# Optimization experiments

Measured on AMD Instinct MI355X. Metric: run time of the kernel, lower is better.

The kernel has to match this reference:

```python
import jax, jax.numpy as jnp
import numpy as np

HEADS = 8

def setup_inputs() -> dict:
    key = jax.random.key(0)
    ks = jax.random.split(key, 6)
    B, HW, C = 8, 1024, 640  # B = b * num_frames, b=1, t=8
    s = 1.0 / np.sqrt(C)
    return {
        "hidden_states": jax.random.normal(ks[0], (B, HW, C), jnp.float32),
        "Wq": jax.random.normal(ks[1], (C, C), jnp.float32) * s,
        "Wk": jax.random.normal(ks[2], (C, C), jnp.float32) * s,
        "Wv": jax.random.normal(ks[3], (C, C), jnp.float32) * s,
        "Wo": jax.random.normal(ks[4], (C, C), jnp.float32) * s,
        "bo": jax.random.normal(ks[5], (C,), jnp.float32) * 0.01,
        "vision_conditon_frames_sample_index": jnp.zeros((1,), jnp.int64 if jax.config.jax_enable_x64 else jnp.int32),
        "num_frames": 8,
    }

def reference(hidden_states, Wq, Wk, Wv, Wo, bo, vision_conditon_frames_sample_index, num_frames):
    B, HW, C = hidden_states.shape
    dh = C // HEADS
    b = B // num_frames
    # (b t) hw c -> b t hw c
    ehs = hidden_states.reshape(b, num_frames, HW, C)
    # gather reference frames: b t_ref hw c -> b 1 (t_ref hw) c, repeat across t
    ip = jnp.take(ehs, vision_conditon_frames_sample_index, axis=1)
    ip = ip.reshape(b, 1, -1, C)
    ip = jnp.broadcast_to(ip, (b, num_frames, ip.shape[2], C))
    # concat per-frame tokens with reference tokens -> (b t) kv c
    ehs = jnp.concatenate([ehs, ip], axis=2).reshape(B, -1, C)
    KV = ehs.shape[1]
    # projections (LoRACompatibleLinear, no bias for q/k/v)
    q = (hidden_states @ Wq).reshape(B, HW, HEADS, dh)
    k = (ehs @ Wk).reshape(B, KV, HEADS, dh)
    v = (ehs @ Wv).reshape(B, KV, HEADS, dh)
    scale = 1.0 / np.sqrt(dh).astype(np.float32)
    logits = jnp.einsum("bqhd,bkhd->bhqk", q, k) * scale
    attn = jax.nn.softmax(logits, axis=-1)
    out = jnp.einsum("bhqk,bkhd->bqhd", attn, v).reshape(B, HW, C)
    # to_out[0] linear (with bias); dropout is identity at inference
    return out @ Wo + bo
```

## Files before the change

kernel.cpp:

```cpp
#include <hip/hip_runtime.h>

typedef __bf16 bf16x8 __attribute__((ext_vector_type(8)));
typedef float  f32x4  __attribute__((ext_vector_type(4)));
typedef unsigned short u16;

#define NFRM 8
#define HW   1024
#define CDIM 640
#define NH   8
#define DH   80

__device__ __forceinline__ u16 bfb(float f) {
    return __builtin_bit_cast(u16, (__bf16)f);
}

__global__ __launch_bounds__(256) void qkv_gemm(
    const float* __restrict__ hs, const float* __restrict__ Wq,
    const float* __restrict__ Wk, const float* __restrict__ Wv,
    u16* __restrict__ Qb, u16* __restrict__ Kb, u16* __restrict__ Vt)
{
    __shared__ u16 Al[128 * 40];
    __shared__ u16 Bl[64 * 40];

    const int m0 = blockIdx.x * 128;
    const int n0 = blockIdx.y * 64;
    const int z  = blockIdx.z;
    const float* __restrict__ W = (z == 0) ? Wq : (z == 1 ? Wk : Wv);

    const int t    = threadIdx.x;
    const int lane = t & 63, w = t >> 6;
    const int wm = w >> 1, wn = w & 1;
    const int g = lane >> 4, l16 = lane & 15;

    f32x4 acc[4][2] = {};

    const int ar = t >> 3;
    const int ac = (t & 7) * 4;

    for (int k0 = 0; k0 < CDIM; k0 += 32) {
        #pragma unroll
        for (int i = 0; i < 4; ++i) {
            int r = ar + i * 32;
            float4 v = *reinterpret_cast<const float4*>(hs + (size_t)(m0 + r) * CDIM + k0 + ac);
            ushort4 u;
            u.x = bfb(v.x); u.y = bfb(v.y); u.z = bfb(v.z); u.w = bfb(v.w);
            *reinterpret_cast<ushort4*>(&Al[r * 40 + ac]) = u;
        }
        #pragma unroll
        for (int i = 0; i < 2; ++i) {
            int nn = ac + i * 32;
            float4 v = *reinterpret_cast<const float4*>(W + (size_t)(k0 + ar) * CDIM + n0 + nn);
            Bl[(nn + 0) * 40 + ar] = bfb(v.x);
            Bl[(nn + 1) * 40 + ar] = bfb(v.y);
            Bl[(nn + 2) * 40 + ar] = bfb(v.z);
            Bl[(nn + 3) * 40 + ar] = bfb(v.w);
        }
        __syncthreads();

        bf16x8 af[4], bfr[2];
        #pragma unroll
        for (int mf = 0; mf < 4; ++mf)
            af[mf] = *reinterpret_cast<const bf16x8*>(&Al[(wm * 64 + mf * 16 + l16) * 40 + g * 8]);
        #pragma unroll
        for (int nf = 0; nf < 2; ++nf)
            bfr[nf] = *reinterpret_cast<const bf16x8*>(&Bl[(wn * 32 + nf * 16 + l16) * 40 + g * 8]);
        #pragma unroll
        for (int mf = 0; mf < 4; ++mf)
            #pragma unroll
            for (int nf = 0; nf < 2; ++nf)
                acc[mf][nf] = __builtin_amdgcn_mfma_f32_16x16x32_bf16(af[mf], bfr[nf], acc[mf][nf], 0, 0, 0);
        __syncthreads();
    }

    #pragma unroll
    for (int mf = 0; mf < 4; ++mf) {
        const int mrow0 = m0 + wm * 64 + mf * 16 + g * 4;
        const int b = mrow0 >> 10, tok0 = mrow0 & 1023;
        #pragma unroll
        for (int nf = 0; nf < 2; ++nf) {
            const int n = n0 + wn * 32 + nf * 16 + l16;
            const int h = n / DH, d = n % DH;
            if (z < 2) {
                u16* dst = (z == 0 ? Qb : Kb);
                size_t base = ((size_t)((b * NH + h) * HW) + tok0) * DH + d;
                #pragma unroll
                for (int rr = 0; rr < 4; ++rr)
                    dst[base + (size_t)rr * DH] = bfb(acc[mf][nf][rr]);
            } else {
                ushort4 u;
                u.x = bfb(acc[mf][nf][0]); u.y = bfb(acc[mf][nf][1]);
                u.z = bfb(acc[mf][nf][2]); u.w = bfb(acc[mf][nf][3]);
                *reinterpret_cast<ushort4*>(&Vt[((size_t)((b * NH + h) * DH) + d) * HW + tok0]) = u;
            }
        }
    }
}

__global__ __launch_bounds__(256) void attn_fwd(
    const u16* __restrict__ Qb, const u16* __restrict__ Kb,
    const u16* __restrict__ Vt, u16* __restrict__ Ob,
    const int* __restrict__ refidx)
{
    __shared__ u16 Kl[64 * 104];
    __shared__ u16 Vl[80 * 72];
    __shared__ u16 Pl[4][16 * 72];

    const int qt = blockIdx.x, h = blockIdx.y, b = blockIdx.z;
    const int t = threadIdx.x, lane = t & 63, w = t >> 6;
    const int g = lane >> 4, l16 = lane & 15;
    const int rfrm = refidx[0];
    const int qbase = qt * 64 + w * 16;

    const int srow = t >> 2;
    const int scol = (t & 3) * 24;

    {
        const u16* src = Qb + ((size_t)((b * NH + h) * HW) + qt * 64 + srow) * DH + scol;
        u16* dst = &Kl[srow * 104 + scol];
        #pragma unroll
        for (int i = 0; i < 3; ++i) {
            const int col = scol + i * 8;
            if (col < DH)
                *reinterpret_cast<uint4*>(dst + i * 8) = *reinterpret_cast<const uint4*>(src + i * 8);
            else
                *reinterpret_cast<uint4*>(dst + i * 8) = uint4{0, 0, 0, 0};
        }
    }
    __syncthreads();
    bf16x8 qf[3];
    #pragma unroll
    for (int s = 0; s < 3; ++s)
        qf[s] = *reinterpret_cast<const bf16x8*>(&Kl[(w * 16 + l16) * 104 + s * 32 + g * 8]);
    __syncthreads();

    float m_i[4], l_i[4];
    #pragma unroll
    for (int rr = 0; rr < 4; ++rr) { m_i[rr] = -1e30f; l_i[rr] = 0.f; }
    f32x4 o[5] = {};
    const float scale = 0.11180339887498948f;

    for (int kt = 0; kt < 32; ++kt) {
        const int fb   = (kt < 16) ? b : rfrm;
        const int tok0 = (kt & 15) * 64;

        {
            const u16* src = Kb + ((size_t)((fb * NH + h) * HW) + tok0 + srow) * DH + scol;
            u16* dst = &Kl[srow * 104 + scol];
            #pragma unroll
            for (int i = 0; i < 3; ++i) {
                const int col = scol + i * 8;
                if (col < DH)
                    *reinterpret_cast<uint4*>(dst + i * 8) = *reinterpret_cast<const uint4*>(src + i * 8);
                else
                    *reinterpret_cast<uint4*>(dst + i * 8) = uint4{0, 0, 0, 0};
            }
        }
        {
            const u16* Vp = Vt + (size_t)((fb * NH + h) * DH) * HW + tok0;
            #pragma unroll
            for (int i = 0; i < 3; ++i) {
                int id = t + i * 256;
                if (id < 640) {
                    int d = id >> 3, c = (id & 7) * 8;
                    *reinterpret_cast<uint4*>(&Vl[d * 72 + c]) =
                        *reinterpret_cast<const uint4*>(Vp + (size_t)d * HW + c);
                }
            }
        }
        __syncthreads();

        f32x4 s4[4] = {};
        #pragma unroll
        for (int nf = 0; nf < 4; ++nf) {
            #pragma unroll
            for (int s = 0; s < 3; ++s) {
                bf16x8 kf = *reinterpret_cast<const bf16x8*>(&Kl[(nf * 16 + l16) * 104 + s * 32 + g * 8]);
                s4[nf] = __builtin_amdgcn_mfma_f32_16x16x32_bf16(qf[s], kf, s4[nf], 0, 0, 0);
            }
        }

        float ps[4][4];
        #pragma unroll
        for (int nf = 0; nf < 4; ++nf)
            #pragma unroll
            for (int rr = 0; rr < 4; ++rr)
                ps[nf][rr] = s4[nf][rr] * scale;

        #pragma unroll
        for (int rr = 0; rr < 4; ++rr) {
            float mx = fmaxf(fmaxf(ps[0][rr], ps[1][rr]), fmaxf(ps[2][rr], ps[3][rr]));
            mx = fmaxf(mx, __shfl_xor(mx, 1));
            mx = fmaxf(mx, __shfl_xor(mx, 2));
            mx = fmaxf(mx, __shfl_xor(mx, 4));
            mx = fmaxf(mx, __shfl_xor(mx, 8));
            const float mnew = fmaxf(m_i[rr], mx);
            const float corr = __expf(m_i[rr] - mnew);
            m_i[rr] = mnew;
            float rsum = 0.f;
            #pragma unroll
            for (int nf = 0; nf < 4; ++nf) {
                float p = __expf(ps[nf][rr] - mnew);
                ps[nf][rr] = p;
                rsum += p;
            }
            rsum += __shfl_xor(rsum, 1);
            rsum += __shfl_xor(rsum, 2);
            rsum += __shfl_xor(rsum, 4);
            rsum += __shfl_xor(rsum, 8);
            l_i[rr] = l_i[rr] * corr + rsum;
            #pragma unroll
            for (int of = 0; of < 5; ++of)
                o[of][rr] = o[of][rr] * corr;
        }

        u16* Pw = &Pl[w][0];
        #pragma unroll
        for (int nf = 0; nf < 4; ++nf)
            #pragma unroll
            for (int rr = 0; rr < 4; ++rr)
                Pw[(g * 4 + rr) * 72 + nf * 16 + l16] = bfb(ps[nf][rr]);

        bf16x8 pa[2];
        #pragma unroll
        for (int ks = 0; ks < 2; ++ks)
            pa[ks] = *reinterpret_cast<const bf16x8*>(&Pw[l16 * 72 + ks * 32 + g * 8]);

        #pragma unroll
        for (int of = 0; of < 5; ++of) {
            #pragma unroll
            for (int ks = 0; ks < 2; ++ks) {
                bf16x8 vf = *reinterpret_cast<const bf16x8*>(&Vl[(of * 16 + l16) * 72 + ks * 32 + g * 8]);
                o[of] = __builtin_amdgcn_mfma_f32_16x16x32_bf16(pa[ks], vf, o[of], 0, 0, 0);
            }
        }
        __syncthreads();
    }

    #pragma unroll
    for (int of = 0; of < 5; ++of) {
        const int d = of * 16 + l16;
        #pragma unroll
        for (int rr = 0; rr < 4; ++rr) {
            const int tok = qbase + g * 4 + rr;
            const float val = o[of][rr] / l_i[rr];
            Ob[((size_t)(b * HW + tok)) * CDIM + h * DH + d] = bfb(val);
        }
    }
}

__global__ __launch_bounds__(256) void out_gemm(
    const u16* __restrict__ A, const float* __restrict__ W,
    const float* __restrict__ bias, float* __restrict__ out)
{
    __shared__ u16 Al[128 * 40];
    __shared__ u16 Bl[64 * 40];

    const int m0 = blockIdx.x * 128;
    const int n0 = blockIdx.y * 64;
    const int t = threadIdx.x;
    const int lane = t & 63, w = t >> 6;
    const int wm = w >> 1, wn = w & 1;
    const int g = lane >> 4, l16 = lane & 15;

    f32x4 acc[4][2] = {};
    const int br = t >> 3;
    const int bc = (t & 7) * 4;

    for (int k0 = 0; k0 < CDIM; k0 += 32) {
        #pragma unroll
        for (int i = 0; i < 2; ++i) {
            int id = t + i * 256;
            int rr = id >> 2, c = (id & 3) * 8;
            *reinterpret_cast<uint4*>(&Al[rr * 40 + c]) =
                *reinterpret_cast<const uint4*>(A + (size_t)(m0 + rr) * CDIM + k0 + c);
        }
        #pragma unroll
        for (int i = 0; i < 2; ++i) {
            int nn = bc + i * 32;
            float4 v = *reinterpret_cast<const float4*>(W + (size_t)(k0 + br) * CDIM + n0 + nn);
            Bl[(nn + 0) * 40 + br] = bfb(v.x);
            Bl[(nn + 1) * 40 + br] = bfb(v.y);
            Bl[(nn + 2) * 40 + br] = bfb(v.z);
            Bl[(nn + 3) * 40 + br] = bfb(v.w);
        }
        __syncthreads();

        bf16x8 af[4], bfr[2];
        #pragma unroll
        for (int mf = 0; mf < 4; ++mf)
            af[mf] = *reinterpret_cast<const bf16x8*>(&Al[(wm * 64 + mf * 16 + l16) * 40 + g * 8]);
        #pragma unroll
        for (int nf = 0; nf < 2; ++nf)
            bfr[nf] = *reinterpret_cast<const bf16x8*>(&Bl[(wn * 32 + nf * 16 + l16) * 40 + g * 8]);
        #pragma unroll
        for (int mf = 0; mf < 4; ++mf)
            #pragma unroll
            for (int nf = 0; nf < 2; ++nf)
                acc[mf][nf] = __builtin_amdgcn_mfma_f32_16x16x32_bf16(af[mf], bfr[nf], acc[mf][nf], 0, 0, 0);
        __syncthreads();
    }

    #pragma unroll
    for (int mf = 0; mf < 4; ++mf) {
        const int mrow0 = m0 + wm * 64 + mf * 16 + g * 4;
        #pragma unroll
        for (int nf = 0; nf < 2; ++nf) {
            const int n = n0 + wn * 32 + nf * 16 + l16;
            const float bs = bias[n];
            #pragma unroll
            for (int rr = 0; rr < 4; ++rr)
                out[(size_t)(mrow0 + rr) * CDIM + n] = acc[mf][nf][rr] + bs;
        }
    }
}

extern "C" void kernel_launch(void* const* d_in, const int* in_sizes, int n_in,
                              void* d_out, int out_size, void* d_ws, size_t ws_size,
                              hipStream_t stream) {
    const float* hs = (const float*)d_in[0];
    const float* Wq = (const float*)d_in[1];
    const float* Wk = (const float*)d_in[2];
    const float* Wv = (const float*)d_in[3];
    const float* Wo = (const float*)d_in[4];
    const float* bo = (const float*)d_in[5];
    const int*   ri = (const int*)d_in[6];
    float* out = (float*)d_out;

    const size_t QKV_ELEMS = (size_t)NFRM * NH * HW * DH;
    u16* Qb = (u16*)d_ws;
    u16* Kb = Qb + QKV_ELEMS;
    u16* Vt = Kb + QKV_ELEMS;
    u16* Ob = Vt + QKV_ELEMS;

    qkv_gemm<<<dim3(64, 10, 3), 256, 0, stream>>>(hs, Wq, Wk, Wv, Qb, Kb, Vt);
    attn_fwd<<<dim3(16, NH, NFRM), 256, 0, stream>>>(Qb, Kb, Vt, Ob, ri);
    out_gemm<<<dim3(64, 10), 256, 0, stream>>>(Ob, Wo, bo, out);
}
```

Measured before the change: 221.9 us.

## Double query tile per attention block and prefetch K/V tiles through registers

```diff
diff --git a/kernel.cpp b/kernel.cpp
--- a/kernel.cpp
+++ b/kernel.cpp
@@ -96,154 +96,178 @@
     }
 }
 
-__global__ __launch_bounds__(256) void attn_fwd(
+__global__ __launch_bounds__(256, 2) void attn_fwd(
     const u16* __restrict__ Qb, const u16* __restrict__ Kb,
     const u16* __restrict__ Vt, u16* __restrict__ Ob,
     const int* __restrict__ refidx)
 {
     __shared__ u16 Kl[64 * 104];
     __shared__ u16 Vl[80 * 72];
-    __shared__ u16 Pl[4][16 * 72];
+    __shared__ u16 Pl[4][32 * 72];
 
     const int qt = blockIdx.x, h = blockIdx.y, b = blockIdx.z;
     const int t = threadIdx.x, lane = t & 63, w = t >> 6;
     const int g = lane >> 4, l16 = lane & 15;
     const int rfrm = refidx[0];
-    const int qbase = qt * 64 + w * 16;
+    const int qbase = qt * 128 + w * 32;
 
     const int srow = t >> 2;
     const int scol = (t & 3) * 24;
 
-    {
-        const u16* src = Qb + ((size_t)((b * NH + h) * HW) + qt * 64 + srow) * DH + scol;
+    bf16x8 qf[2][3];
+    #pragma unroll
+    for (int mf = 0; mf < 2; ++mf) {
+        const u16* Qp = Qb + ((size_t)((b * NH + h) * HW) + qbase + mf * 16 + l16) * DH;
+        qf[mf][0] = *reinterpret_cast<const bf16x8*>(Qp + g * 8);
+        qf[mf][1] = *reinterpret_cast<const bf16x8*>(Qp + 32 + g * 8);
+        if (g < 2) qf[mf][2] = *reinterpret_cast<const bf16x8*>(Qp + 64 + g * 8);
+        else       qf[mf][2] = (bf16x8)((__bf16)0.f);
+    }
+
+    int vd[3], vc[3];
+    bool vv[3];
+    #pragma unroll
+    for (int i = 0; i < 3; ++i) {
+        int id = t + i * 256;
+        vv[i] = id < 640;
+        vd[i] = id >> 3;
+        vc[i] = (id & 7) * 8;
+    }
+
+    uint4 kreg[3], vreg[3];
+    auto load_kv = [&](int kt2) {
+        const int fb   = (kt2 < 16) ? b : rfrm;
+        const int tok0 = (kt2 & 15) * 64;
+        const u16* ks = Kb + ((size_t)((fb * NH + h) * HW) + tok0 + srow) * DH + scol;
+        #pragma unroll
+        for (int i = 0; i < 3; ++i)
+            kreg[i] = *reinterpret_cast<const uint4*>(ks + i * 8);
+        const u16* vs = Vt + ((size_t)(fb * NH + h) * DH) * HW + tok0;
+        #pragma unroll
+        for (int i = 0; i < 3; ++i)
+            if (vv[i]) vreg[i] = *reinterpret_cast<const uint4*>(vs + (size_t)vd[i] * HW + vc[i]);
+    };
+    auto store_kv = [&]() {
         u16* dst = &Kl[srow * 104 + scol];
         #pragma unroll
         for (int i = 0; i < 3; ++i) {
-            const int col = scol + i * 8;
-            if (col < DH)
-                *reinterpret_cast<uint4*>(dst + i * 8) = *reinterpret_cast<const uint4*>(src + i * 8);
-            else
-                *reinterpret_cast<uint4*>(dst + i * 8) = uint4{0, 0, 0, 0};
-        }
-    }
-    __syncthreads();
-    bf16x8 qf[3];
-    #pragma unroll
-    for (int s = 0; s < 3; ++s)
-        qf[s] = *reinterpret_cast<const bf16x8*>(&Kl[(w * 16 + l16) * 104 + s * 32 + g * 8]);
-    __syncthreads();
-
-    float m_i[4], l_i[4];
-    #pragma unroll
-    for (int rr = 0; rr < 4; ++rr) { m_i[rr] = -1e30f; l_i[rr] = 0.f; }
-    f32x4 o[5] = {};
+            const uint4 z4 = {0, 0, 0, 0};
+            *reinterpret_cast<uint4*>(dst + i * 8) = (scol + i * 8 < DH) ? kreg[i] : z4;
+        }
+        #pragma unroll
+        for (int i = 0; i < 3; ++i)
+            if (vv[i]) *reinterpret_cast<uint4*>(&Vl[vd[i] * 72 + vc[i]]) = vreg[i];
+    };
+
+    load_kv(0);
+    store_kv();
+
+    float m_i[2][4], l_i[2][4];
+    #pragma unroll
+    for (int mf = 0; mf < 2; ++mf)
+        #pragma unroll
+        for (int rr = 0; rr < 4; ++rr) { m_i[mf][rr] = -1e30f; l_i[mf][rr] = 0.f; }
+    f32x4 o[2][5] = {};
     const float scale = 0.11180339887498948f;
 
     for (int kt = 0; kt < 32; ++kt) {
-        const int fb   = (kt < 16) ? b : rfrm;
-        const int tok0 = (kt & 15) * 64;
-
-        {
-            const u16* src = Kb + ((size_t)((fb * NH + h) * HW) + tok0 + srow) * DH + scol;
-            u16* dst = &Kl[srow * 104 + scol];
-            #pragma unroll
-            for (int i = 0; i < 3; ++i) {
-                const int col = scol + i * 8;
-                if (col < DH)
-                    *reinterpret_cast<uint4*>(dst + i * 8) = *reinterpret_cast<const uint4*>(src + i * 8);
-                else
-                    *reinterpret_cast<uint4*>(dst + i * 8) = uint4{0, 0, 0, 0};
-            }
-        }
-        {
-            const u16* Vp = Vt + (size_t)((fb * NH + h) * DH) * HW + tok0;
-            #pragma unroll
-            for (int i = 0; i < 3; ++i) {
-                int id = t + i * 256;
-                if (id < 640) {
-                    int d = id >> 3, c = (id & 7) * 8;
-                    *reinterpret_cast<uint4*>(&Vl[d * 72 + c]) =
-                        *reinterpret_cast<const uint4*>(Vp + (size_t)d * HW + c);
+        __syncthreads();
+        if (kt < 31) load_kv(kt + 1);
+
+        f32x4 s4[2][4] = {};
+        #pragma unroll
+        for (int s = 0; s < 3; ++s) {
+            #pragma unroll
+            for (int nf = 0; nf < 4; ++nf) {
+                bf16x8 kf = *reinterpret_cast<const bf16x8*>(&Kl[(nf * 16 + l16) * 104 + s * 32 + g * 8]);
+                s4[0][nf] = __builtin_amdgcn_mfma_f32_16x16x32_bf16(qf[0][s], kf, s4[0][nf], 0, 0, 0);
+                s4[1][nf] = __builtin_amdgcn_mfma_f32_16x16x32_bf16(qf[1][s], kf, s4[1][nf], 0, 0, 0);
+            }
+        }
+
+        float ps[2][4][4];
+        #pragma unroll
+        for (int mf = 0; mf < 2; ++mf)
+            #pragma unroll
+            for (int nf = 0; nf < 4; ++nf)
+                #pragma unroll
+                for (int rr = 0; rr < 4; ++rr)
+                    ps[mf][nf][rr] = s4[mf][nf][rr] * scale;
+
+        #pragma unroll
+        for (int mf = 0; mf < 2; ++mf) {
+            #pragma unroll
+            for (int rr = 0; rr < 4; ++rr) {
+                float mx = fmaxf(fmaxf(ps[mf][0][rr], ps[mf][1][rr]),
+                                 fmaxf(ps[mf][2][rr], ps[mf][3][rr]));
+                mx = fmaxf(mx, __shfl_xor(mx, 1));
+                mx = fmaxf(mx, __shfl_xor(mx, 2));
+                mx = fmaxf(mx, __shfl_xor(mx, 4));
+                mx = fmaxf(mx, __shfl_xor(mx, 8));
+                if (mx > m_i[mf][rr]) {
+                    const float corr = __expf(m_i[mf][rr] - mx);
+                    m_i[mf][rr] = mx;
+                    l_i[mf][rr] *= corr;
+                    #pragma unroll
+                    for (int of = 0; of < 5; ++of)
+                        o[mf][of][rr] *= corr;
                 }
-            }
-        }
-        __syncthreads();
-
-        f32x4 s4[4] = {};
-        #pragma unroll
-        for (int nf = 0; nf < 4; ++nf) {
-            #pragma unroll
-            for (int s = 0; s < 3; ++s) {
-                bf16x8 kf = *reinterpret_cast<const bf16x8*>(&Kl[(nf * 16 + l16) * 104 + s * 32 + g * 8]);
-                s4[nf] = __builtin_amdgcn_mfma_f32_16x16x32_bf16(qf[s], kf, s4[nf], 0, 0, 0);
-            }
-        }
-
-        float ps[4][4];
-        #pragma unroll
-        for (int nf = 0; nf < 4; ++nf)
-            #pragma unroll
-            for (int rr = 0; rr < 4; ++rr)
-                ps[nf][rr] = s4[nf][rr] * scale;
-
-        #pragma unroll
-        for (int rr = 0; rr < 4; ++rr) {
-            float mx = fmaxf(fmaxf(ps[0][rr], ps[1][rr]), fmaxf(ps[2][rr], ps[3][rr]));
-            mx = fmaxf(mx, __shfl_xor(mx, 1));
-            mx = fmaxf(mx, __shfl_xor(mx, 2));
-            mx = fmaxf(mx, __shfl_xor(mx, 4));
-            mx = fmaxf(mx, __shfl_xor(mx, 8));
-            const float mnew = fmaxf(m_i[rr], mx);
-            const float corr = __expf(m_i[rr] - mnew);
-            m_i[rr] = mnew;
-            float rsum = 0.f;
-            #pragma unroll
-            for (int nf = 0; nf < 4; ++nf) {
-                float p = __expf(ps[nf][rr] - mnew);
-                ps[nf][rr] = p;
-                rsum += p;
-            }
-            rsum += __shfl_xor(rsum, 1);
-            rsum += __shfl_xor(rsum, 2);
-            rsum += __shfl_xor(rsum, 4);
-            rsum += __shfl_xor(rsum, 8);
-            l_i[rr] = l_i[rr] * corr + rsum;
-            #pragma unroll
-            for (int of = 0; of < 5; ++of)
-                o[of][rr] = o[of][rr] * corr;
+                const float mnew = m_i[mf][rr];
+                float rsum = 0.f;
+                #pragma unroll
+                for (int nf = 0; nf < 4; ++nf) {
+                    float p = __expf(ps[mf][nf][rr] - mnew);
+                    ps[mf][nf][rr] = p;
+                    rsum += p;
+                }
+                rsum += __shfl_xor(rsum, 1);
+                rsum += __shfl_xor(rsum, 2);
+                rsum += __shfl_xor(rsum, 4);
+                rsum += __shfl_xor(rsum, 8);
+                l_i[mf][rr] += rsum;
+            }
         }
 
         u16* Pw = &Pl[w][0];
         #pragma unroll
-        for (int nf = 0; nf < 4; ++nf)
-            #pragma unroll
-            for (int rr = 0; rr < 4; ++rr)
-                Pw[(g * 4 + rr) * 72 + nf * 16 + l16] = bfb(ps[nf][rr]);
-
-        bf16x8 pa[2];
-        #pragma unroll
-        for (int ks = 0; ks < 2; ++ks)
-            pa[ks] = *reinterpret_cast<const bf16x8*>(&Pw[l16 * 72 + ks * 32 + g * 8]);
+        for (int mf = 0; mf < 2; ++mf)
+            #pragma unroll
+            for (int nf = 0; nf < 4; ++nf)
+                #pragma unroll
+                for (int rr = 0; rr < 4; ++rr)
+                    Pw[(mf * 16 + g * 4 + rr) * 72 + nf * 16 + l16] = bfb(ps[mf][nf][rr]);
+
+        bf16x8 pa[2][2];
+        #pragma unroll
+        for (int mf = 0; mf < 2; ++mf)
+            #pragma unroll
+            for (int ks = 0; ks < 2; ++ks)
+                pa[mf][ks] = *reinterpret_cast<const bf16x8*>(&Pw[(mf * 16 + l16) * 72 + ks * 32 + g * 8]);
 
         #pragma unroll
         for (int of = 0; of < 5; ++of) {
             #pragma unroll
             for (int ks = 0; ks < 2; ++ks) {
                 bf16x8 vf = *reinterpret_cast<const bf16x8*>(&Vl[(of * 16 + l16) * 72 + ks * 32 + g * 8]);
-                o[of] = __builtin_amdgcn_mfma_f32_16x16x32_bf16(pa[ks], vf, o[of], 0, 0, 0);
-            }
-        }
-        __syncthreads();
-    }
-
-    #pragma unroll
-    for (int of = 0; of < 5; ++of) {
-        const int d = of * 16 + l16;
-        #pragma unroll
-        for (int rr = 0; rr < 4; ++rr) {
-            const int tok = qbase + g * 4 + rr;
-            const float val = o[of][rr] / l_i[rr];
-            Ob[((size_t)(b * HW + tok)) * CDIM + h * DH + d] = bfb(val);
+                o[0][of] = __builtin_amdgcn_mfma_f32_16x16x32_bf16(pa[0][ks], vf, o[0][of], 0, 0, 0);
+                o[1][of] = __builtin_amdgcn_mfma_f32_16x16x32_bf16(pa[1][ks], vf, o[1][of], 0, 0, 0);
+            }
+        }
+        __syncthreads();
+        if (kt < 31) store_kv();
+    }
+
+    #pragma unroll
+    for (int mf = 0; mf < 2; ++mf) {
+        #pragma unroll
+        for (int of = 0; of < 5; ++of) {
+            const int d = of * 16 + l16;
+            #pragma unroll
+            for (int rr = 0; rr < 4; ++rr) {
+                const int tok = qbase + mf * 16 + g * 4 + rr;
+                const float val = o[mf][of][rr] / l_i[mf][rr];
+                Ob[((size_t)(b * HW + tok)) * CDIM + h * DH + d] = bfb(val);
+            }
         }
     }
 }
@@ -333,6 +357,6 @@
     u16* Ob = Vt + QKV_ELEMS;
 
     qkv_gemm<<<dim3(64, 10, 3), 256, 0, stream>>>(hs, Wq, Wk, Wv, Qb, Kb, Vt);
-    attn_fwd<<<dim3(16, NH, NFRM), 256, 0, stream>>>(Qb, Kb, Vt, Ob, ri);
+    attn_fwd<<<dim3(8, NH, NFRM), 256, 0, stream>>>(Qb, Kb, Vt, Ob, ri);
     out_gemm<<<dim3(64, 10), 256, 0, stream>>>(Ob, Wo, bo, out);
 }
```

Result: slower. 278.0 us (+25.3%).

## Prefetch next K/V tile into registers and use exp2 softmax with lazy rescale

Applied to the files above, without the earlier changes.

```diff
diff --git a/kernel.cpp b/kernel.cpp
--- a/kernel.cpp
+++ b/kernel.cpp
@@ -114,66 +114,68 @@
     const int srow = t >> 2;
     const int scol = (t & 3) * 24;
 
+    bf16x8 qf[3];
     {
-        const u16* src = Qb + ((size_t)((b * NH + h) * HW) + qt * 64 + srow) * DH + scol;
+        const u16* Qp = Qb + ((size_t)((b * NH + h) * HW) + qbase + l16) * DH;
+        qf[0] = *reinterpret_cast<const bf16x8*>(Qp + g * 8);
+        qf[1] = *reinterpret_cast<const bf16x8*>(Qp + 32 + g * 8);
+        if (g < 2) qf[2] = *reinterpret_cast<const bf16x8*>(Qp + 64 + g * 8);
+        else       qf[2] = (bf16x8)((__bf16)0.f);
+    }
+
+    int vd[3], vc[3];
+    bool vv[3];
+    #pragma unroll
+    for (int i = 0; i < 3; ++i) {
+        int id = t + i * 256;
+        vv[i] = id < 640;
+        vd[i] = id >> 3;
+        vc[i] = (id & 7) * 8;
+    }
+
+    uint4 kreg[3], vreg[3];
+    auto load_kv = [&](int kt2) {
+        const int fb   = (kt2 < 16) ? b : rfrm;
+        const int tok0 = (kt2 & 15) * 64;
+        const u16* ks = Kb + ((size_t)((fb * NH + h) * HW) + tok0 + srow) * DH + scol;
+        #pragma unroll
+        for (int i = 0; i < 3; ++i)
+            kreg[i] = *reinterpret_cast<const uint4*>(ks + i * 8);
+        const u16* vs = Vt + ((size_t)(fb * NH + h) * DH) * HW + tok0;
+        #pragma unroll
+        for (int i = 0; i < 3; ++i)
+            if (vv[i]) vreg[i] = *reinterpret_cast<const uint4*>(vs + (size_t)vd[i] * HW + vc[i]);
+    };
+    auto store_kv = [&]() {
         u16* dst = &Kl[srow * 104 + scol];
         #pragma unroll
         for (int i = 0; i < 3; ++i) {
-            const int col = scol + i * 8;
-            if (col < DH)
-                *reinterpret_cast<uint4*>(dst + i * 8) = *reinterpret_cast<const uint4*>(src + i * 8);
-            else
-                *reinterpret_cast<uint4*>(dst + i * 8) = uint4{0, 0, 0, 0};
-        }
-    }
-    __syncthreads();
-    bf16x8 qf[3];
-    #pragma unroll
-    for (int s = 0; s < 3; ++s)
-        qf[s] = *reinterpret_cast<const bf16x8*>(&Kl[(w * 16 + l16) * 104 + s * 32 + g * 8]);
-    __syncthreads();
+            const uint4 z4 = {0, 0, 0, 0};
+            *reinterpret_cast<uint4*>(dst + i * 8) = (scol + i * 8 < DH) ? kreg[i] : z4;
+        }
+        #pragma unroll
+        for (int i = 0; i < 3; ++i)
+            if (vv[i]) *reinterpret_cast<uint4*>(&Vl[vd[i] * 72 + vc[i]]) = vreg[i];
+    };
+
+    load_kv(0);
+    store_kv();
 
     float m_i[4], l_i[4];
     #pragma unroll
     for (int rr = 0; rr < 4; ++rr) { m_i[rr] = -1e30f; l_i[rr] = 0.f; }
     f32x4 o[5] = {};
-    const float scale = 0.11180339887498948f;
+    const float scale2 = 0.11180339887498948f * 1.4426950408889634f;
 
     for (int kt = 0; kt < 32; ++kt) {
-        const int fb   = (kt < 16) ? b : rfrm;
-        const int tok0 = (kt & 15) * 64;
-
-        {
-            const u16* src = Kb + ((size_t)((fb * NH + h) * HW) + tok0 + srow) * DH + scol;
-            u16* dst = &Kl[srow * 104 + scol];
-            #pragma unroll
-            for (int i = 0; i < 3; ++i) {
-                const int col = scol + i * 8;
-                if (col < DH)
-                    *reinterpret_cast<uint4*>(dst + i * 8) = *reinterpret_cast<const uint4*>(src + i * 8);
-                else
-                    *reinterpret_cast<uint4*>(dst + i * 8) = uint4{0, 0, 0, 0};
-            }
-        }
-        {
-            const u16* Vp = Vt + (size_t)((fb * NH + h) * DH) * HW + tok0;
-            #pragma unroll
-            for (int i = 0; i < 3; ++i) {
-                int id = t + i * 256;
-                if (id < 640) {
-                    int d = id >> 3, c = (id & 7) * 8;
-                    *reinterpret_cast<uint4*>(&Vl[d * 72 + c]) =
-                        *reinterpret_cast<const uint4*>(Vp + (size_t)d * HW + c);
-                }
-            }
-        }
-        __syncthreads();
+        __syncthreads();
+        if (kt < 31) load_kv(kt + 1);
 
         f32x4 s4[4] = {};
         #pragma unroll
-        for (int nf = 0; nf < 4; ++nf) {
-            #pragma unroll
-            for (int s = 0; s < 3; ++s) {
+        for (int s = 0; s < 3; ++s) {
+            #pragma unroll
+            for (int nf = 0; nf < 4; ++nf) {
                 bf16x8 kf = *reinterpret_cast<const bf16x8*>(&Kl[(nf * 16 + l16) * 104 + s * 32 + g * 8]);
                 s4[nf] = __builtin_amdgcn_mfma_f32_16x16x32_bf16(qf[s], kf, s4[nf], 0, 0, 0);
             }
@@ -184,7 +186,7 @@
         for (int nf = 0; nf < 4; ++nf)
             #pragma unroll
             for (int rr = 0; rr < 4; ++rr)
-                ps[nf][rr] = s4[nf][rr] * scale;
+                ps[nf][rr] = s4[nf][rr] * scale2;
 
         #pragma unroll
         for (int rr = 0; rr < 4; ++rr) {
@@ -193,13 +195,19 @@
             mx = fmaxf(mx, __shfl_xor(mx, 2));
             mx = fmaxf(mx, __shfl_xor(mx, 4));
             mx = fmaxf(mx, __shfl_xor(mx, 8));
-            const float mnew = fmaxf(m_i[rr], mx);
-            const float corr = __expf(m_i[rr] - mnew);
-            m_i[rr] = mnew;
+            if (mx > m_i[rr]) {
+                const float corr = exp2f(m_i[rr] - mx);
+                m_i[rr] = mx;
+                l_i[rr] *= corr;
+                #pragma unroll
+                for (int of = 0; of < 5; ++of)
+                    o[of][rr] *= corr;
+            }
+            const float mnew = m_i[rr];
             float rsum = 0.f;
             #pragma unroll
             for (int nf = 0; nf < 4; ++nf) {
-                float p = __expf(ps[nf][rr] - mnew);
+                float p = exp2f(ps[nf][rr] - mnew);
                 ps[nf][rr] = p;
                 rsum += p;
             }
@@ -207,10 +215,7 @@
             rsum += __shfl_xor(rsum, 2);
             rsum += __shfl_xor(rsum, 4);
             rsum += __shfl_xor(rsum, 8);
-            l_i[rr] = l_i[rr] * corr + rsum;
-            #pragma unroll
-            for (int of = 0; of < 5; ++of)
-                o[of][rr] = o[of][rr] * corr;
+            l_i[rr] += rsum;
         }
 
         u16* Pw = &Pl[w][0];
@@ -234,6 +239,7 @@
             }
         }
         __syncthreads();
+        if (kt < 31) store_kv();
     }
 
     #pragma unroll
```

After: 436.7 us. 96.8% more time.
